# Performance work log

Hardware: AMD Instinct MI355X
Metric: run time of the kernel (lower is better)

The kernel has to match this reference:

```python
import jax, jax.numpy as jnp
import numpy as np

B, E, L, D = 64, 32, 512, 768
C1 = 1024
C2 = 1024
H = 8
EG = 32768
SPAN_H = 512
NLAB = 4


def setup_inputs() -> dict:
    key = jax.random.key(0)
    ks = jax.random.split(key, 48)
    def w(i, shape, s=0.02):
        return s * jax.random.normal(ks[i], shape, jnp.float32)
    N = B * E
    inp = {}
    inp['last_hidden'] = jax.random.normal(ks[0], (B, L, D), jnp.float32)
    mask = (jax.random.uniform(ks[1], (B, E, L)) < 0.25).astype(jnp.float32)
    inp['batch_edu_mask'] = mask.at[:, :, 0].set(1.0)  # every EDU has >=1 token
    inp['edu_lengths'] = jax.random.randint(ks[2], (B,), 1, E + 1)
    inp['batch_edge'] = jax.random.randint(ks[3], (2, EG), 0, N)
    inp['batch_edge_type'] = jax.random.randint(ks[4], (EG, 1), 0, 5).astype(jnp.float32)
    inp['batch_is_main'] = jax.random.randint(ks[5], (EG, 1), 0, 2).astype(jnp.float32)
    # span attention MLP
    inp['W1'] = w(6, (D, SPAN_H)); inp['b1'] = jnp.zeros((SPAN_H,), jnp.float32)
    inp['W2'] = w(7, (SPAN_H, 1)); inp['b2'] = jnp.zeros((1,), jnp.float32)
    # edge-attr embeddings (Linear(1, C))
    inp['Wr1'] = w(8, (1, C1)); inp['br1'] = jnp.zeros((C1,), jnp.float32)
    inp['Wm1'] = w(9, (1, C1)); inp['bm1'] = jnp.zeros((C1,), jnp.float32)
    inp['Wr2'] = w(10, (1, C2)); inp['br2'] = jnp.zeros((C2,), jnp.float32)
    inp['Wm2'] = w(11, (1, C2)); inp['bm2'] = jnp.zeros((C2,), jnp.float32)
    # TransformerConv 1: in=D, heads*out=C1, edge_dim=C1
    inp['q1W'] = w(12, (D, C1)); inp['q1b'] = jnp.zeros((C1,), jnp.float32)
    inp['k1W'] = w(13, (D, C1)); inp['k1b'] = jnp.zeros((C1,), jnp.float32)
    inp['v1W'] = w(14, (D, C1)); inp['v1b'] = jnp.zeros((C1,), jnp.float32)
    inp['e1W'] = w(15, (C1, C1))
    inp['s1W'] = w(16, (D, C1)); inp['s1b'] = jnp.zeros((C1,), jnp.float32)
    # TransformerConv 2: in=C1, heads*out=C2, edge_dim=C2
    inp['q2W'] = w(17, (C1, C2)); inp['q2b'] = jnp.zeros((C2,), jnp.float32)
    inp['k2W'] = w(18, (C1, C2)); inp['k2b'] = jnp.zeros((C2,), jnp.float32)
    inp['v2W'] = w(19, (C1, C2)); inp['v2b'] = jnp.zeros((C2,), jnp.float32)
    inp['e2W'] = w(20, (C2, C2))
    inp['s2W'] = w(21, (C1, C2)); inp['s2b'] = jnp.zeros((C2,), jnp.float32)
    inp['fcW'] = w(22, (C2, NLAB)); inp['fcb'] = jnp.zeros((NLAB,), jnp.float32)
    return inp


def _tconv(x, src, dst, edge_attr, Wq, bq, Wk, bk, Wv, bv, We, Ws, bs):
    # PyG TransformerConv (concat=True, beta=False, root_weight=True)
    N = x.shape[0]
    C = Wq.shape[1]
    d = C // H
    q = (x @ Wq + bq).reshape(N, H, d)              # [N,H,d]
    e = (edge_attr @ We).reshape(-1, H, d)          # [Eg,H,d] (lin_edge has no bias)
    k = (x @ Wk + bk)[src].reshape(-1, H, d) + e    # [Eg,H,d]
    v = (x @ Wv + bv)[src].reshape(-1, H, d) + e    # [Eg,H,d]
    logits = (q[dst] * k).sum(-1) / jnp.sqrt(jnp.float32(d))  # [Eg,H]
    m = jax.ops.segment_max(logits, dst, num_segments=N)
    ex = jnp.exp(logits - m[dst])
    den = jax.ops.segment_sum(ex, dst, num_segments=N)
    alpha = ex / den[dst]                            # scatter-softmax over dst
    agg = jax.ops.segment_sum(v * alpha[:, :, None], dst, num_segments=N).reshape(N, C)
    return agg + x @ Ws + bs                         # skip connection


def reference(last_hidden, batch_edu_mask, edu_lengths, batch_edge, batch_edge_type, batch_is_main,
              W1, b1, W2, b2,
              Wr1, br1, Wm1, bm1, Wr2, br2, Wm2, bm2,
              q1W, q1b, k1W, k1b, v1W, v1b, e1W, s1W, s1b,
              q2W, q2b, k2W, k2b, v2W, v2b, e2W, s2W, s2b,
              fcW, fcb):
    b = last_hidden.shape[0]
    # span extractor: masked softmax attention pooling per EDU
    att = jnp.maximum(last_hidden @ W1 + b1, 0.0) @ W2 + b2      # [B,L,1]
    logits = jnp.swapaxes(att, 1, 2) - 1e5 * (1.0 - batch_edu_mask)  # [B,E,L]
    probs = jax.nn.softmax(logits, axis=-1)
    edu = probs @ last_hidden                                     # [B,E,D]
    node = edu.reshape(-1, edu.shape[-1])                         # [B*E,D]
    src, dst = batch_edge[0], batch_edge[1]
    ea1 = batch_edge_type @ Wr1 + br1 + batch_is_main @ Wm1 + bm1
    node = _tconv(node, src, dst, ea1, q1W, q1b, k1W, k1b, v1W, v1b, e1W, s1W, s1b)
    ea2 = batch_edge_type @ Wr2 + br2 + batch_is_main @ Wm2 + bm2
    node = _tconv(node, src, dst, ea2, q2W, q2b, k2W, k2b, v2W, v2b, e2W, s2W, s2b)
    node = node.reshape(b, -1, node.shape[-1])                    # [B,E,C2]
    last_du = node[jnp.arange(b), edu_lengths - 1]                # [B,C2]
    return last_du @ fcW + fcb                                    # [B,NLAB]
```

## Files before the change

### kernel.cpp

```cpp
#include <hip/hip_runtime.h>
#include <math.h>
#include <stdint.h>

#define B_  64
#define E_  32
#define L_  512
#define D_  768
#define C_  1024
#define H_  8
#define EG_ 32768
#define SH_ 512
#define N_  2048
#define ND_ (N_ * D_)

typedef __bf16 bf16x8 __attribute__((ext_vector_type(8)));
typedef float f32x4 __attribute__((ext_vector_type(4)));
typedef unsigned short u16;
typedef u16 u16x4 __attribute__((ext_vector_type(4)));


__device__ __forceinline__ u16 bf16_rn(float x) {
  unsigned u = __builtin_bit_cast(unsigned, x);
  unsigned r = u + 0x7FFFu + ((u >> 16) & 1u);
  return (u16)(r >> 16);
}

__device__ __forceinline__ void gload16(const void* g, void* l) {
  __builtin_amdgcn_global_load_lds(
      (const __attribute__((address_space(1))) void*)(unsigned long long)(uintptr_t)g,
      (__attribute__((address_space(3))) void*)(unsigned int)(uintptr_t)l,
      16, 0, 0);
}

__global__ void k_wt9(const float* __restrict__ s0, const float* __restrict__ s1,
                      const float* __restrict__ s2, const float* __restrict__ s3,
                      const float* __restrict__ s4, const float* __restrict__ s5,
                      const float* __restrict__ s6, const float* __restrict__ s7,
                      const float* __restrict__ s8, u16* __restrict__ dstBase) {
  int x = blockIdx.x;
  const float* W; u16* TH; int K, Nc;
  if (x < 384) {
    W = s0; TH = dstBase; K = D_; Nc = SH_;
  } else if (x < 384 + 4 * 768) {
    int i = (x - 384) / 768; x = (x - 384) % 768;
    W = (i == 0) ? s1 : (i == 1) ? s2 : (i == 2) ? s3 : s4;
    TH = dstBase + SH_ * D_ + (size_t)i * C_ * D_; K = D_; Nc = C_;
  } else {
    int i = (x - 3456) / 1024; x = (x - 3456) % 1024;
    W = (i == 0) ? s5 : (i == 1) ? s6 : (i == 2) ? s7 : s8;
    TH = dstBase + SH_ * D_ + 4 * (size_t)C_ * D_ + (size_t)i * C_ * C_; K = C_; Nc = C_;
  }
  __shared__ float Ts[32][33];
  int nbk = K >> 5;
  int bk = x % nbk, bn = x / nbk;
  int tid = threadIdx.x;
  int tx = tid & 31, ty = tid >> 5;
  for (int r = ty; r < 32; r += 8)
    Ts[r][tx] = W[(size_t)(bk * 32 + r) * Nc + bn * 32 + tx];
  __syncthreads();
  for (int r = ty; r < 32; r += 8) {
    float v = Ts[tx][r];
    TH[(size_t)(bn * 32 + r) * K + bk * 32 + tx] = bf16_rn(v);
  }
}

__device__ __forceinline__ void gemm_core(
    const float* __restrict__ X, const u16* __restrict__ Bt,
    int K, int row0, int col0,
    u16* Ah, u16* Bh, f32x4 acc[4][4])
{
  int tid = threadIdx.x;
  int lane = tid & 63, w = tid >> 6;

  int aoff[4], boff[4];
#pragma unroll
  for (int i = 0; i < 4; i++) {
    int kc = lane >> 4;
    int rT = (w & 1) * 64 + i * 16 + (lane & 15);
    aoff[i] = rT * 128 + (((kc ^ (rT & 7)) & 7) << 4);
    int cT = (w >> 1) * 64 + i * 16 + (lane & 15);
    boff[i] = cT * 128 + (((kc ^ (cT & 7)) & 7) << 4);
  }

  int nkt = K >> 6;
  for (int kt = 0; kt < nkt; kt++) {
    int k0 = kt << 6;
    if (kt) __syncthreads();
#pragma unroll
    for (int p = 0; p < 8; p++) {
      int idx = tid + p * 256;
      int r = idx >> 4, c4 = idx & 15;
      float4 v = *(const float4*)&X[(size_t)(row0 + r) * K + k0 + c4 * 4];
      u16x4 hv = {bf16_rn(v.x), bf16_rn(v.y), bf16_rn(v.z), bf16_rn(v.w)};
      int off = r * 128 + ((((c4 >> 1) ^ (r & 7)) & 7) << 4) + (c4 & 1) * 8;
      *(u16x4*)((char*)Ah + off) = hv;
    }
#pragma unroll
    for (int q = 0; q < 4; q++) {
      int rT = w * 32 + q * 8 + (lane >> 3);
      int cs = (lane & 7) ^ (rT & 7);
      size_t gb = (size_t)(col0 + rT) * K + k0 + cs * 8;
      int lb = (w * 32 + q * 8) * 64;
      gload16(&Bt[gb], &Bh[lb]);
    }
    __syncthreads();
    bf16x8 ah0[4], ah1[4];
#pragma unroll
    for (int i = 0; i < 4; i++) {
      ah0[i] = *(const bf16x8*)((const char*)Ah + aoff[i]);
      ah1[i] = *(const bf16x8*)((const char*)Ah + (aoff[i] ^ 64));
    }
#pragma unroll
    for (int j = 0; j < 4; j++) {
      bf16x8 bh0 = *(const bf16x8*)((const char*)Bh + boff[j]);
#pragma unroll
      for (int i = 0; i < 4; i++)
        acc[i][j] = __builtin_amdgcn_mfma_f32_16x16x32_bf16(ah0[i], bh0, acc[i][j], 0, 0, 0);
      bf16x8 bh1 = *(const bf16x8*)((const char*)Bh + (boff[j] ^ 64));
#pragma unroll
      for (int i = 0; i < 4; i++)
        acc[i][j] = __builtin_amdgcn_mfma_f32_16x16x32_bf16(ah1[i], bh1, acc[i][j], 0, 0, 0);
    }
  }
}

__global__ __launch_bounds__(512, 2) void k_span_m(
    const float* __restrict__ lh, const u16* __restrict__ W1t,
    const float* __restrict__ b1, const float* __restrict__ W2,
    float* __restrict__ att) {
  __shared__ __align__(16) u16 Ah[64 * 64];
  __shared__ __align__(16) u16 Bh[512 * 64];
  int row0 = blockIdx.x * 64;
  int tid = threadIdx.x, lane = tid & 63, w = tid >> 6;

  f32x4 acc[4][4];
#pragma unroll
  for (int i = 0; i < 4; i++)
#pragma unroll
    for (int j = 0; j < 4; j++) acc[i][j] = (f32x4){0.f, 0.f, 0.f, 0.f};

  int kc = lane >> 4;
  int aoff[4], boff[4];
#pragma unroll
  for (int i = 0; i < 4; i++) {
    int rT = i * 16 + (lane & 15);
    aoff[i] = rT * 128 + (((kc ^ (rT & 7)) & 7) << 4);
  }
#pragma unroll
  for (int j = 0; j < 4; j++) {
    int cT = w * 64 + j * 16 + (lane & 15);
    boff[j] = cT * 128 + (((kc ^ (cT & 7)) & 7) << 4);
  }

  for (int kt = 0; kt < 12; kt++) {
    int k0 = kt << 6;
    if (kt) __syncthreads();
#pragma unroll
    for (int p = 0; p < 2; p++) {
      int idx = tid + p * 512;
      int r = idx >> 4, c4 = idx & 15;
      float4 v = *(const float4*)&lh[(size_t)(row0 + r) * D_ + k0 + c4 * 4];
      u16x4 hv = {bf16_rn(v.x), bf16_rn(v.y), bf16_rn(v.z), bf16_rn(v.w)};
      int off = r * 128 + ((((c4 >> 1) ^ (r & 7)) & 7) << 4) + (c4 & 1) * 8;
      *(u16x4*)((char*)Ah + off) = hv;
    }
#pragma unroll
    for (int q = 0; q < 8; q++) {
      int rT = w * 64 + q * 8 + (lane >> 3);
      int cs = (lane & 7) ^ (rT & 7);
      size_t gb = (size_t)rT * D_ + k0 + cs * 8;
      int lb = (w * 64 + q * 8) * 64;
      gload16(&W1t[gb], &Bh[lb]);
    }
    __syncthreads();
    bf16x8 ah0[4], ah1[4];
#pragma unroll
    for (int i = 0; i < 4; i++) {
      ah0[i] = *(const bf16x8*)((const char*)Ah + aoff[i]);
      ah1[i] = *(const bf16x8*)((const char*)Ah + (aoff[i] ^ 64));
    }
#pragma unroll
    for (int j = 0; j < 4; j++) {
      bf16x8 bh0 = *(const bf16x8*)((const char*)Bh + boff[j]);
#pragma unroll
      for (int i = 0; i < 4; i++)
        acc[i][j] = __builtin_amdgcn_mfma_f32_16x16x32_bf16(ah0[i], bh0, acc[i][j], 0, 0, 0);
      bf16x8 bh1 = *(const bf16x8*)((const char*)Bh + (boff[j] ^ 64));
#pragma unroll
      for (int i = 0; i < 4; i++)
        acc[i][j] = __builtin_amdgcn_mfma_f32_16x16x32_bf16(ah1[i], bh1, acc[i][j], 0, 0, 0);
    }
  }

  float b1v[4], w2v[4];
#pragma unroll
  for (int j = 0; j < 4; j++) {
    int col = w * 64 + j * 16 + (lane & 15);
    b1v[j] = b1[col]; w2v[j] = W2[col];
  }
  __syncthreads();
  float* sred = (float*)Ah;
#pragma unroll
  for (int i = 0; i < 4; i++) {
#pragma unroll
    for (int r = 0; r < 4; r++) {
      float s = 0.f;
#pragma unroll
      for (int j = 0; j < 4; j++) {
        float h = acc[i][j][r] + b1v[j];
        s += fmaxf(h, 0.f) * w2v[j];
      }
      s += __shfl_xor(s, 1); s += __shfl_xor(s, 2);
      s += __shfl_xor(s, 4); s += __shfl_xor(s, 8);
      if ((lane & 15) == 0)
        sred[w * 64 + i * 16 + (lane >> 4) * 4 + r] = s;
    }
  }
  __syncthreads();
  if (tid < 64) {
    float s = 0.f;
#pragma unroll
    for (int p = 0; p < 8; p++) s += sred[p * 64 + tid];
    att[row0 + tid] = s;
  }
}

__global__ void k_probs(const float* __restrict__ att, const float* __restrict__ b2,
                        const float* __restrict__ mask, float* __restrict__ pr) {
  int bi = blockIdx.x >> 2, eg = blockIdx.x & 3;
  int tid = threadIdx.x, lane = tid & 63, w = tid >> 6;
  __shared__ float att_s[512];
  float b2v = b2[0];
  int r0 = bi * 512 + tid;
  att_s[tid] = att[r0] + b2v;
  att_s[tid + 256] = att[r0 + 256] + b2v;
  __syncthreads();
#pragma unroll
  for (int it = 0; it < 2; it++) {
    int e = eg * 8 + it * 4 + w;
    const float* mrow = &mask[(size_t)(bi * E_ + e) * L_];
    float4 m0 = *(const float4*)&mrow[lane * 8];
    float4 m1 = *(const float4*)&mrow[lane * 8 + 4];
    float4 a0 = *(const float4*)&att_s[lane * 8];
    float4 a1 = *(const float4*)&att_s[lane * 8 + 4];
    float v[8];
    v[0] = a0.x - 1e5f * (1.f - m0.x); v[1] = a0.y - 1e5f * (1.f - m0.y);
    v[2] = a0.z - 1e5f * (1.f - m0.z); v[3] = a0.w - 1e5f * (1.f - m0.w);
    v[4] = a1.x - 1e5f * (1.f - m1.x); v[5] = a1.y - 1e5f * (1.f - m1.y);
    v[6] = a1.z - 1e5f * (1.f - m1.z); v[7] = a1.w - 1e5f * (1.f - m1.w);
    float mx = v[0];
#pragma unroll
    for (int i = 1; i < 8; i++) mx = fmaxf(mx, v[i]);
#pragma unroll
    for (int o = 32; o; o >>= 1) mx = fmaxf(mx, __shfl_xor(mx, o));
    float s = 0.f;
#pragma unroll
    for (int i = 0; i < 8; i++) { v[i] = expf(v[i] - mx); s += v[i]; }
#pragma unroll
    for (int o = 32; o; o >>= 1) s += __shfl_xor(s, o);
    float inv = 1.f / s;
    float4 o0 = {v[0] * inv, v[1] * inv, v[2] * inv, v[3] * inv};
    float4 o1 = {v[4] * inv, v[5] * inv, v[6] * inv, v[7] * inv};
    float* prow = &pr[(size_t)(bi * E_ + e) * L_];
    *(float4*)&prow[lane * 8] = o0;
    *(float4*)&prow[lane * 8 + 4] = o1;
  }
}

__global__ __launch_bounds__(256) void k_pool_m(const float* __restrict__ lh,
    const float* __restrict__ pr, float* __restrict__ node0) {
  __shared__ __align__(16) u16 As[32 * 32];
  __shared__ __align__(16) u16 Bs[32 * 128];
  int bi = blockIdx.x / 6, dc = blockIdx.x % 6;
  int col0 = dc * 128;
  int tid = threadIdx.x, lane = tid & 63, w = tid >> 6;
  const float* lhb = lh + (size_t)bi * L_ * D_;
  const float* prb = pr + (size_t)bi * E_ * L_;

  f32x4 acc[2][2];
#pragma unroll
  for (int m = 0; m < 2; m++)
#pragma unroll
    for (int c = 0; c < 2; c++) acc[m][c] = (f32x4){0.f, 0.f, 0.f, 0.f};

  int aoff[2];
#pragma unroll
  for (int m = 0; m < 2; m++) {
    int kc = lane >> 4;
    int e = m * 16 + (lane & 15);
    aoff[m] = e * 64 + (((kc ^ ((e >> 1) & 3)) & 3) << 4);
  }
  int se = tid >> 3, sk4 = tid & 7;
  int saoff = se * 64 + ((((sk4 >> 1) ^ ((se >> 1) & 3)) & 3) << 4) + (sk4 & 1) * 8;

  for (int kt = 0; kt < 16; kt++) {
    int l0 = kt << 5;
    if (kt) __syncthreads();
    {
      float4 v = *(const float4*)&prb[(size_t)se * L_ + l0 + sk4 * 4];
      u16x4 hv = {bf16_rn(v.x), bf16_rn(v.y), bf16_rn(v.z), bf16_rn(v.w)};
      *(u16x4*)((char*)As + saoff) = hv;
    }
#pragma unroll
    for (int p = 0; p < 4; p++) {
      int idx = tid + p * 256;
      int k = idx >> 5, c4 = idx & 31;
      float4 v = *(const float4*)&lhb[(size_t)(l0 + k) * D_ + col0 + c4 * 4];
      u16x4 hv = {bf16_rn(v.x), bf16_rn(v.y), bf16_rn(v.z), bf16_rn(v.w)};
      *(u16x4*)&Bs[k * 128 + c4 * 4] = hv;
    }
    __syncthreads();
    bf16x8 af[2];
#pragma unroll
    for (int m = 0; m < 2; m++)
      af[m] = *(const bf16x8*)((const char*)As + aoff[m]);
#pragma unroll
    for (int c = 0; c < 2; c++) {
      int colT = w * 32 + c * 16 + (lane & 15);
      int kg = (lane >> 4) * 8;
      union { bf16x8 v; u16 u[8]; } bb;
#pragma unroll
      for (int j = 0; j < 8; j++) bb.u[j] = Bs[(kg + j) * 128 + colT];
#pragma unroll
      for (int m = 0; m < 2; m++)
        acc[m][c] = __builtin_amdgcn_mfma_f32_16x16x32_bf16(af[m], bb.v, acc[m][c], 0, 0, 0);
    }
  }
#pragma unroll
  for (int m = 0; m < 2; m++)
#pragma unroll
    for (int c = 0; c < 2; c++) {
      int col = col0 + w * 32 + c * 16 + (lane & 15);
#pragma unroll
      for (int r = 0; r < 4; r++) {
        int e = m * 16 + (lane >> 4) * 4 + r;
        node0[(size_t)(bi * E_ + e) * D_ + col] = acc[m][c][r];
      }
    }
}

__global__ __launch_bounds__(256) void k_gemm4_m(
    const float* __restrict__ X, int K,
    const u16* __restrict__ Wt,
    const float* __restrict__ bb0, const float* __restrict__ bb1,
    const float* __restrict__ bb2, const float* __restrict__ bb3,
    float* __restrict__ O0, float* __restrict__ O1,
    float* __restrict__ O2, float* __restrict__ O3) {
  __shared__ __align__(16) u16 Ah[128 * 64], Bh[128 * 64];
  int rb = blockIdx.x & 15, cbm = blockIdx.x >> 4;
  int mat = cbm >> 3;
  int col0 = (cbm & 7) * 128, row0 = rb * 128;
  const u16* Bt = Wt + (size_t)mat * C_ * K;
  const float* bias; float* O;
  if (mat == 0)      { bias = bb0; O = O0; }
  else if (mat == 1) { bias = bb1; O = O1; }
  else if (mat == 2) { bias = bb2; O = O2; }
  else               { bias = bb3; O = O3; }

  f32x4 acc[4][4];
#pragma unroll
  for (int i = 0; i < 4; i++)
#pragma unroll
    for (int j = 0; j < 4; j++) acc[i][j] = (f32x4){0.f, 0.f, 0.f, 0.f};
  gemm_core(X, Bt, K, row0, col0, Ah, Bh, acc);

  int lane = threadIdx.x & 63, w = threadIdx.x >> 6;
  int wrow = (w & 1) * 64, wcol = (w >> 1) * 64;
#pragma unroll
  for (int j = 0; j < 4; j++) {
    int col = col0 + wcol + j * 16 + (lane & 15);
    float bv = bias[col];
#pragma unroll
    for (int i = 0; i < 4; i++) {
      int rowb = row0 + wrow + i * 16 + (lane >> 4) * 4;
#pragma unroll
      for (int r = 0; r < 4; r++)
        O[(size_t)(rowb + r) * C_ + col] = acc[i][j][r] + bv;
    }
  }
}

__global__ void k_combo2(const float* __restrict__ Wr1, const float* __restrict__ br1,
                         const float* __restrict__ Wm1, const float* __restrict__ bm1,
                         const float* __restrict__ e1W,
                         const float* __restrict__ Wr2, const float* __restrict__ br2,
                         const float* __restrict__ Wm2, const float* __restrict__ bm2,
                         const float* __restrict__ e2W,
                         float* __restrict__ e1c, float* __restrict__ e2c) {
  int x = blockIdx.x;
  int conv = x >> 6;
  int jb = x & 3, kb = (x >> 2) & 15;
  const float *Wr, *br, *Wm, *bm, *eW; float* out;
  if (conv == 0) { Wr = Wr1; br = br1; Wm = Wm1; bm = bm1; eW = e1W; out = e1c; }
  else           { Wr = Wr2; br = br2; Wm = Wm2; bm = bm2; eW = e2W; out = e2c; }
  int tid = threadIdx.x;
  __shared__ float sw[3][64];
  int k0 = kb * 64;
  if (tid < 64) {
    sw[0][tid] = Wr[k0 + tid];
    sw[1][tid] = Wm[k0 + tid];
    sw[2][tid] = br[k0 + tid] + bm[k0 + tid];
  }
  __syncthreads();
  int j = jb * 256 + tid;
  float a0 = 0.f, a1 = 0.f, a2 = 0.f;
#pragma unroll 8
  for (int kk = 0; kk < 64; kk++) {
    float w = eW[(size_t)(k0 + kk) * C_ + j];
    a0 += sw[0][kk] * w; a1 += sw[1][kk] * w; a2 += sw[2][kk] * w;
  }
#pragma unroll
  for (int c = 0; c < 10; c++)
    atomicAdd(&out[c * C_ + j], (float)(c >> 1) * a0 + (float)(c & 1) * a1 + a2);
}

__global__ void k_count(const int* __restrict__ dst, int* __restrict__ cnt) {
  int eg = blockIdx.x * 256 + threadIdx.x;
  atomicAdd(&cnt[dst[eg]], 1);
}

__global__ void k_scan(const int* __restrict__ cnt, int* __restrict__ off) {
  __shared__ int part[256];
  int t = threadIdx.x;
  int local[8]; int s = 0;
#pragma unroll
  for (int i = 0; i < 8; i++) { local[i] = cnt[t * 8 + i]; s += local[i]; }
  part[t] = s;
  __syncthreads();
  if (t == 0) {
    int r = 0;
    for (int i = 0; i < 256; i++) { int v = part[i]; part[i] = r; r += v; }
    off[N_] = r;
  }
  __syncthreads();
  int r = part[t];
#pragma unroll
  for (int i = 0; i < 8; i++) { off[t * 8 + i] = r; r += local[i]; }
}

__global__ void k_scatter(const int* __restrict__ dst, int* __restrict__ wcnt,
                          const int* __restrict__ off, int* __restrict__ perm) {
  int eg = blockIdx.x * 256 + threadIdx.x;
  int d = dst[eg];
  int p = atomicAdd(&wcnt[d], 1);
  perm[off[d] + p] = eg;
}

__global__ void k_agg(const float* __restrict__ q, const float* __restrict__ k,
                      const float* __restrict__ v, const float* __restrict__ ec,
                      const int* __restrict__ srcA, const float* __restrict__ etype,
                      const float* __restrict__ emain, const int* __restrict__ off,
                      const int* __restrict__ perm, float* __restrict__ O) {
  int dst = blockIdx.x;
  int beg = off[dst];
  int cntE = off[dst + 1] - beg;
  if (cntE == 0) return;
  if (cntE > 128) cntE = 128;
  int tid = threadIdx.x;
  __shared__ float lg[128][8];
  __shared__ int srcs[128];
  __shared__ int cids[128];
  for (int e = tid; e < cntE; e += 256) {
    int eg = perm[beg + e];
    srcs[e] = srcA[eg];
    cids[e] = ((int)(etype[eg] + 0.5f)) * 2 + (int)(emain[eg] + 0.5f);
  }
  __syncthreads();
  int c = tid * 4;
  int h = tid >> 5;
  float4 qv = *(const float4*)&q[dst * C_ + c];
  const float scale = 0.08838834764831845f;
  for (int e = 0; e < cntE; e++) {
    int s = srcs[e], ci = cids[e];
    float4 kv = *(const float4*)&k[s * C_ + c];
    float4 ev = *(const float4*)&ec[ci * C_ + c];
    float p = qv.x * (kv.x + ev.x) + qv.y * (kv.y + ev.y) +
              qv.z * (kv.z + ev.z) + qv.w * (kv.w + ev.w);
#pragma unroll
    for (int o = 16; o; o >>= 1) p += __shfl_xor(p, o);
    if ((tid & 31) == 0) lg[e][h] = p * scale;
  }
  __syncthreads();
  if (tid < 8) {
    float m = -1e30f;
    for (int e = 0; e < cntE; e++) m = fmaxf(m, lg[e][tid]);
    float ssum = 0.f;
    for (int e = 0; e < cntE; e++) { float x = expf(lg[e][tid] - m); lg[e][tid] = x; ssum += x; }
    float inv = 1.f / ssum;
    for (int e = 0; e < cntE; e++) lg[e][tid] *= inv;
  }
  __syncthreads();
  float4 acc = {0.f, 0.f, 0.f, 0.f};
  for (int e = 0; e < cntE; e++) {
    float a = lg[e][h];
    int s = srcs[e], ci = cids[e];
    float4 vv = *(const float4*)&v[s * C_ + c];
    float4 ev = *(const float4*)&ec[ci * C_ + c];
    acc.x += a * (vv.x + ev.x); acc.y += a * (vv.y + ev.y);
    acc.z += a * (vv.z + ev.z); acc.w += a * (vv.w + ev.w);
  }
  float4 o = *(const float4*)&O[dst * C_ + c];
  o.x += acc.x; o.y += acc.y; o.z += acc.z; o.w += acc.w;
  *(float4*)&O[dst * C_ + c] = o;
}

__global__ void k_final(const float* __restrict__ nB, const int* __restrict__ lens,
                        const float* __restrict__ fcW, const float* __restrict__ fcb,
                        float* __restrict__ out) {
  int b = blockIdx.x;
  int idx = lens[b] - 1;
  const float* row = &nB[(b * E_ + idx) * C_];
  int tid = threadIdx.x;
  int c = tid * 4;
  float4 r = *(const float4*)&row[c];
  float4 w0 = *(const float4*)&fcW[(c + 0) * 4];
  float4 w1 = *(const float4*)&fcW[(c + 1) * 4];
  float4 w2 = *(const float4*)&fcW[(c + 2) * 4];
  float4 w3 = *(const float4*)&fcW[(c + 3) * 4];
  float p0 = r.x * w0.x + r.y * w1.x + r.z * w2.x + r.w * w3.x;
  float p1 = r.x * w0.y + r.y * w1.y + r.z * w2.y + r.w * w3.y;
  float p2 = r.x * w0.z + r.y * w1.z + r.z * w2.z + r.w * w3.z;
  float p3 = r.x * w0.w + r.y * w1.w + r.z * w2.w + r.w * w3.w;
#pragma unroll
  for (int o = 32; o; o >>= 1) {
    p0 += __shfl_xor(p0, o); p1 += __shfl_xor(p1, o);
    p2 += __shfl_xor(p2, o); p3 += __shfl_xor(p3, o);
  }
  __shared__ float red[4][4];
  if ((tid & 63) == 0) {
    int w = tid >> 6;
    red[w][0] = p0; red[w][1] = p1; red[w][2] = p2; red[w][3] = p3;
  }
  __syncthreads();
  if (tid == 0) {
#pragma unroll
    for (int j = 0; j < 4; j++)
      out[b * 4 + j] = red[0][j] + red[1][j] + red[2][j] + red[3][j] + fcb[j];
  }
}

extern "C" void kernel_launch(void* const* d_in, const int* in_sizes, int n_in,
                              void* d_out, int out_size, void* d_ws, size_t ws_size,
                              hipStream_t stream) {
  (void)in_sizes; (void)n_in; (void)out_size; (void)ws_size;
  const float* lh    = (const float*)d_in[0];
  const float* mask  = (const float*)d_in[1];
  const int*   lens  = (const int*)d_in[2];
  const int*   edge  = (const int*)d_in[3];
  const float* etype = (const float*)d_in[4];
  const float* emain = (const float*)d_in[5];
  const float* W1   = (const float*)d_in[6];
  const float* b1   = (const float*)d_in[7];
  const float* W2   = (const float*)d_in[8];
  const float* b2   = (const float*)d_in[9];
  const float* Wr1  = (const float*)d_in[10];
  const float* br1  = (const float*)d_in[11];
  const float* Wm1  = (const float*)d_in[12];
  const float* bm1  = (const float*)d_in[13];
  const float* Wr2  = (const float*)d_in[14];
  const float* br2  = (const float*)d_in[15];
  const float* Wm2  = (const float*)d_in[16];
  const float* bm2  = (const float*)d_in[17];
  const float* q1W  = (const float*)d_in[18];
  const float* q1b  = (const float*)d_in[19];
  const float* k1W  = (const float*)d_in[20];
  const float* k1b  = (const float*)d_in[21];
  const float* v1W  = (const float*)d_in[22];
  const float* v1b  = (const float*)d_in[23];
  const float* e1W  = (const float*)d_in[24];
  const float* s1W  = (const float*)d_in[25];
  const float* s1b  = (const float*)d_in[26];
  const float* q2W  = (const float*)d_in[27];
  const float* q2b  = (const float*)d_in[28];
  const float* k2W  = (const float*)d_in[29];
  const float* k2b  = (const float*)d_in[30];
  const float* v2W  = (const float*)d_in[31];
  const float* v2b  = (const float*)d_in[32];
  const float* e2W  = (const float*)d_in[33];
  const float* s2W  = (const float*)d_in[34];
  const float* s2b  = (const float*)d_in[35];
  const float* fcW  = (const float*)d_in[36];
  const float* fcb  = (const float*)d_in[37];

  float* ws    = (float*)d_ws;
  float* att   = ws;
  float* node0 = att + 32768;
  float* e1c   = node0 + ND_;
  float* e2c   = e1c + 10 * 1024;
  float* qb    = e2c + 10 * 1024;
  float* kb    = qb + N_ * C_;
  float* vb    = kb + N_ * C_;
  float* nA    = vb + N_ * C_;
  float* nBuf  = nA + N_ * C_;
  int* cnt  = (int*)(nBuf + N_ * C_);
  int* wcnt = cnt + N_;
  int* off  = wcnt + N_;
  int* perm = off + (N_ + 8);
  u16* wtb  = (u16*)(perm + EG_);
  u16* w1t  = wtb;
  u16* wt1  = w1t + SH_ * D_;
  u16* wt2  = wt1 + 4 * C_ * D_;

  float* pr   = qb;

  const int* srcA = edge;
  const int* dstA = edge + EG_;

  (void)hipMemsetAsync(cnt, 0, 2 * N_ * sizeof(int), stream);
  k_count<<<EG_ / 256, 256, 0, stream>>>(dstA, cnt);
  k_scan<<<1, 256, 0, stream>>>(cnt, off);
  k_scatter<<<EG_ / 256, 256, 0, stream>>>(dstA, wcnt, off, perm);

  k_wt9<<<384 + 4 * 768 + 4 * 1024, 256, 0, stream>>>(
      W1, q1W, k1W, v1W, s1W, q2W, k2W, v2W, s2W, wtb);

  k_span_m<<<512, 512, 0, stream>>>(lh, w1t, b1, W2, att);

  (void)hipMemsetAsync(e1c, 0, 20 * C_ * sizeof(float), stream);
  k_combo2<<<128, 256, 0, stream>>>(Wr1, br1, Wm1, bm1, e1W,
                                    Wr2, br2, Wm2, bm2, e2W, e1c, e2c);

  k_probs<<<256, 256, 0, stream>>>(att, b2, mask, pr);
  k_pool_m<<<384, 256, 0, stream>>>(lh, pr, node0);

  k_gemm4_m<<<512, 256, 0, stream>>>(node0, D_, wt1,
                                     q1b, k1b, v1b, s1b, qb, kb, vb, nA);
  k_agg<<<N_, 256, 0, stream>>>(qb, kb, vb, e1c, srcA, etype, emain, off, perm, nA);

  k_gemm4_m<<<512, 256, 0, stream>>>(nA, C_, wt2,
                                     q2b, k2b, v2b, s2b, qb, kb, vb, nBuf);
  k_agg<<<N_, 256, 0, stream>>>(qb, kb, vb, e2c, srcA, etype, emain, off, perm, nBuf);

  k_final<<<B_, 256, 0, stream>>>(nBuf, lens, fcW, fcb, (float*)d_out);
}
```

Measured before the change: 244.5 us.

## Store Q/K/V in bf16 and retile span GEMM into row/column halves

The Q/K/V projections are now written as bf16, and the edge-aggregation kernel reads them as bf16 and widens to float. This halves the bytes of the irregular gathers over source nodes. The span-attention GEMM now gives each block 128 rows by 256 columns instead of 64 rows by all 512, with two partial score buffers summed in k_probs. That cuts shared memory per block and raises the occupancy target to 6. The trade-off is extra rounding error in the attention logits and values.

```diff
diff --git a/kernel.cpp b/kernel.cpp
--- a/kernel.cpp
+++ b/kernel.cpp
@@ -23,6 +23,10 @@
   unsigned u = __builtin_bit_cast(unsigned, x);
   unsigned r = u + 0x7FFFu + ((u >> 16) & 1u);
   return (u16)(r >> 16);
+}
+
+__device__ __forceinline__ float bf2f(u16 u) {
+  return __builtin_bit_cast(float, (unsigned)u << 16);
 }
 
 __device__ __forceinline__ void gload16(const void* g, void* l) {
@@ -124,14 +128,16 @@
   }
 }
 
-__global__ __launch_bounds__(512, 2) void k_span_m(
+__global__ __launch_bounds__(512, 6) void k_span_m(
     const float* __restrict__ lh, const u16* __restrict__ W1t,
     const float* __restrict__ b1, const float* __restrict__ W2,
-    float* __restrict__ att) {
-  __shared__ __align__(16) u16 Ah[64 * 64];
-  __shared__ __align__(16) u16 Bh[512 * 64];
-  int row0 = blockIdx.x * 64;
+    float* __restrict__ att2) {
+  __shared__ __align__(16) u16 Ah[128 * 64];
+  __shared__ __align__(16) u16 Bh[256 * 64];
+  int rb = blockIdx.x >> 1, cb = blockIdx.x & 1;
+  int row0 = rb * 128, col0 = cb * 256;
   int tid = threadIdx.x, lane = tid & 63, w = tid >> 6;
+  int rh = w & 1, cq = w >> 1;
 
   f32x4 acc[4][4];
 #pragma unroll
@@ -143,12 +149,12 @@
   int aoff[4], boff[4];
 #pragma unroll
   for (int i = 0; i < 4; i++) {
-    int rT = i * 16 + (lane & 15);
+    int rT = rh * 64 + i * 16 + (lane & 15);
     aoff[i] = rT * 128 + (((kc ^ (rT & 7)) & 7) << 4);
   }
 #pragma unroll
   for (int j = 0; j < 4; j++) {
-    int cT = w * 64 + j * 16 + (lane & 15);
+    int cT = cq * 64 + j * 16 + (lane & 15);
     boff[j] = cT * 128 + (((kc ^ (cT & 7)) & 7) << 4);
   }
 
@@ -156,7 +162,7 @@
     int k0 = kt << 6;
     if (kt) __syncthreads();
 #pragma unroll
-    for (int p = 0; p < 2; p++) {
+    for (int p = 0; p < 4; p++) {
       int idx = tid + p * 512;
       int r = idx >> 4, c4 = idx & 15;
       float4 v = *(const float4*)&lh[(size_t)(row0 + r) * D_ + k0 + c4 * 4];
@@ -165,11 +171,11 @@
       *(u16x4*)((char*)Ah + off) = hv;
     }
 #pragma unroll
-    for (int q = 0; q < 8; q++) {
-      int rT = w * 64 + q * 8 + (lane >> 3);
+    for (int q = 0; q < 4; q++) {
+      int rT = w * 32 + q * 8 + (lane >> 3);
       int cs = (lane & 7) ^ (rT & 7);
-      size_t gb = (size_t)rT * D_ + k0 + cs * 8;
-      int lb = (w * 64 + q * 8) * 64;
+      size_t gb = (size_t)(col0 + rT) * D_ + k0 + cs * 8;
+      int lb = (w * 32 + q * 8) * 64;
       gload16(&W1t[gb], &Bh[lb]);
     }
     __syncthreads();
@@ -195,7 +201,7 @@
   float b1v[4], w2v[4];
 #pragma unroll
   for (int j = 0; j < 4; j++) {
-    int col = w * 64 + j * 16 + (lane & 15);
+    int col = col0 + cq * 64 + j * 16 + (lane & 15);
     b1v[j] = b1[col]; w2v[j] = W2[col];
   }
   __syncthreads();
@@ -213,27 +219,24 @@
       s += __shfl_xor(s, 1); s += __shfl_xor(s, 2);
       s += __shfl_xor(s, 4); s += __shfl_xor(s, 8);
       if ((lane & 15) == 0)
-        sred[w * 64 + i * 16 + (lane >> 4) * 4 + r] = s;
-    }
-  }
-  __syncthreads();
-  if (tid < 64) {
-    float s = 0.f;
-#pragma unroll
-    for (int p = 0; p < 8; p++) s += sred[p * 64 + tid];
-    att[row0 + tid] = s;
-  }
-}
-
-__global__ void k_probs(const float* __restrict__ att, const float* __restrict__ b2,
+        sred[cq * 128 + rh * 64 + i * 16 + (lane >> 4) * 4 + r] = s;
+    }
+  }
+  __syncthreads();
+  if (tid < 128)
+    att2[(size_t)cb * 32768 + row0 + tid] =
+        sred[tid] + sred[128 + tid] + sred[256 + tid] + sred[384 + tid];
+}
+
+__global__ void k_probs(const float* __restrict__ att2, const float* __restrict__ b2,
                         const float* __restrict__ mask, float* __restrict__ pr) {
   int bi = blockIdx.x >> 2, eg = blockIdx.x & 3;
   int tid = threadIdx.x, lane = tid & 63, w = tid >> 6;
   __shared__ float att_s[512];
   float b2v = b2[0];
   int r0 = bi * 512 + tid;
-  att_s[tid] = att[r0] + b2v;
-  att_s[tid + 256] = att[r0 + 256] + b2v;
+  att_s[tid]       = att2[r0] + att2[32768 + r0] + b2v;
+  att_s[tid + 256] = att2[r0 + 256] + att2[32768 + r0 + 256] + b2v;
   __syncthreads();
 #pragma unroll
   for (int it = 0; it < 2; it++) {
@@ -344,18 +347,18 @@
     const u16* __restrict__ Wt,
     const float* __restrict__ bb0, const float* __restrict__ bb1,
     const float* __restrict__ bb2, const float* __restrict__ bb3,
-    float* __restrict__ O0, float* __restrict__ O1,
-    float* __restrict__ O2, float* __restrict__ O3) {
+    u16* __restrict__ O0, u16* __restrict__ O1,
+    u16* __restrict__ O2, float* __restrict__ O3) {
   __shared__ __align__(16) u16 Ah[128 * 64], Bh[128 * 64];
   int rb = blockIdx.x & 15, cbm = blockIdx.x >> 4;
   int mat = cbm >> 3;
   int col0 = (cbm & 7) * 128, row0 = rb * 128;
   const u16* Bt = Wt + (size_t)mat * C_ * K;
-  const float* bias; float* O;
-  if (mat == 0)      { bias = bb0; O = O0; }
-  else if (mat == 1) { bias = bb1; O = O1; }
-  else if (mat == 2) { bias = bb2; O = O2; }
-  else               { bias = bb3; O = O3; }
+  const float* bias;
+  if (mat == 0)      bias = bb0;
+  else if (mat == 1) bias = bb1;
+  else if (mat == 2) bias = bb2;
+  else               bias = bb3;
 
   f32x4 acc[4][4];
 #pragma unroll
@@ -366,16 +369,32 @@
 
   int lane = threadIdx.x & 63, w = threadIdx.x >> 6;
   int wrow = (w & 1) * 64, wcol = (w >> 1) * 64;
-#pragma unroll
-  for (int j = 0; j < 4; j++) {
-    int col = col0 + wcol + j * 16 + (lane & 15);
-    float bv = bias[col];
-#pragma unroll
-    for (int i = 0; i < 4; i++) {
-      int rowb = row0 + wrow + i * 16 + (lane >> 4) * 4;
-#pragma unroll
-      for (int r = 0; r < 4; r++)
-        O[(size_t)(rowb + r) * C_ + col] = acc[i][j][r] + bv;
+  if (mat < 3) {
+    u16* O = (mat == 0) ? O0 : (mat == 1) ? O1 : O2;
+#pragma unroll
+    for (int j = 0; j < 4; j++) {
+      int col = col0 + wcol + j * 16 + (lane & 15);
+      float bv = bias[col];
+#pragma unroll
+      for (int i = 0; i < 4; i++) {
+        int rowb = row0 + wrow + i * 16 + (lane >> 4) * 4;
+#pragma unroll
+        for (int r = 0; r < 4; r++)
+          O[(size_t)(rowb + r) * C_ + col] = bf16_rn(acc[i][j][r] + bv);
+      }
+    }
+  } else {
+#pragma unroll
+    for (int j = 0; j < 4; j++) {
+      int col = col0 + wcol + j * 16 + (lane & 15);
+      float bv = bias[col];
+#pragma unroll
+      for (int i = 0; i < 4; i++) {
+        int rowb = row0 + wrow + i * 16 + (lane >> 4) * 4;
+#pragma unroll
+        for (int r = 0; r < 4; r++)
+          O3[(size_t)(rowb + r) * C_ + col] = acc[i][j][r] + bv;
+      }
     }
   }
 }
@@ -446,8 +465,8 @@
   perm[off[d] + p] = eg;
 }
 
-__global__ void k_agg(const float* __restrict__ q, const float* __restrict__ k,
-                      const float* __restrict__ v, const float* __restrict__ ec,
+__global__ void k_agg(const u16* __restrict__ q, const u16* __restrict__ k,
+                      const u16* __restrict__ v, const float* __restrict__ ec,
                       const int* __restrict__ srcA, const float* __restrict__ etype,
                       const float* __restrict__ emain, const int* __restrict__ off,
                       const int* __restrict__ perm, float* __restrict__ O) {
@@ -468,14 +487,15 @@
   __syncthreads();
   int c = tid * 4;
   int h = tid >> 5;
-  float4 qv = *(const float4*)&q[dst * C_ + c];
+  ushort4 q4 = *(const ushort4*)&q[(size_t)dst * C_ + c];
+  float qx = bf2f(q4.x), qy = bf2f(q4.y), qz = bf2f(q4.z), qw = bf2f(q4.w);
   const float scale = 0.08838834764831845f;
   for (int e = 0; e < cntE; e++) {
     int s = srcs[e], ci = cids[e];
-    float4 kv = *(const float4*)&k[s * C_ + c];
+    ushort4 k4 = *(const ushort4*)&k[(size_t)s * C_ + c];
     float4 ev = *(const float4*)&ec[ci * C_ + c];
-    float p = qv.x * (kv.x + ev.x) + qv.y * (kv.y + ev.y) +
-              qv.z * (kv.z + ev.z) + qv.w * (kv.w + ev.w);
+    float p = qx * (bf2f(k4.x) + ev.x) + qy * (bf2f(k4.y) + ev.y) +
+              qz * (bf2f(k4.z) + ev.z) + qw * (bf2f(k4.w) + ev.w);
 #pragma unroll
     for (int o = 16; o; o >>= 1) p += __shfl_xor(p, o);
     if ((tid & 31) == 0) lg[e][h] = p * scale;
@@ -494,14 +514,14 @@
   for (int e = 0; e < cntE; e++) {
     float a = lg[e][h];
     int s = srcs[e], ci = cids[e];
-    float4 vv = *(const float4*)&v[s * C_ + c];
+    ushort4 v4 = *(const ushort4*)&v[(size_t)s * C_ + c];
     float4 ev = *(const float4*)&ec[ci * C_ + c];
-    acc.x += a * (vv.x + ev.x); acc.y += a * (vv.y + ev.y);
-    acc.z += a * (vv.z + ev.z); acc.w += a * (vv.w + ev.w);
-  }
-  float4 o = *(const float4*)&O[dst * C_ + c];
+    acc.x += a * (bf2f(v4.x) + ev.x); acc.y += a * (bf2f(v4.y) + ev.y);
+    acc.z += a * (bf2f(v4.z) + ev.z); acc.w += a * (bf2f(v4.w) + ev.w);
+  }
+  float4 o = *(const float4*)&O[(size_t)dst * C_ + c];
   o.x += acc.x; o.y += acc.y; o.z += acc.z; o.w += acc.w;
-  *(float4*)&O[dst * C_ + c] = o;
+  *(float4*)&O[(size_t)dst * C_ + c] = o;
 }
 
 __global__ void k_final(const float* __restrict__ nB, const int* __restrict__ lens,
@@ -583,25 +603,25 @@
   const float* fcb  = (const float*)d_in[37];
 
   float* ws    = (float*)d_ws;
-  float* att   = ws;
-  float* node0 = att + 32768;
+  float* node0 = ws + 32768;
   float* e1c   = node0 + ND_;
   float* e2c   = e1c + 10 * 1024;
-  float* qb    = e2c + 10 * 1024;
-  float* kb    = qb + N_ * C_;
-  float* vb    = kb + N_ * C_;
-  float* nA    = vb + N_ * C_;
-  float* nBuf  = nA + N_ * C_;
-  int* cnt  = (int*)(nBuf + N_ * C_);
+  u16* qb16 = (u16*)(e2c + 10 * 1024);
+  u16* kb16 = qb16 + (size_t)N_ * C_;
+  u16* vb16 = kb16 + (size_t)N_ * C_;
+  float* nA   = (float*)(vb16 + (size_t)N_ * C_);
+  float* nBuf = nA + (size_t)N_ * C_;
+  int* cnt  = (int*)(nBuf + (size_t)N_ * C_);
   int* wcnt = cnt + N_;
   int* off  = wcnt + N_;
   int* perm = off + (N_ + 8);
   u16* wtb  = (u16*)(perm + EG_);
   u16* w1t  = wtb;
   u16* wt1  = w1t + SH_ * D_;
-  u16* wt2  = wt1 + 4 * C_ * D_;
-
-  float* pr   = qb;
+  u16* wt2  = wt1 + 4 * (size_t)C_ * D_;
+
+  float* pr   = (float*)qb16;
+  float* att2 = (float*)kb16;
 
   const int* srcA = edge;
   const int* dstA = edge + EG_;
@@ -614,22 +634,22 @@
   k_wt9<<<384 + 4 * 768 + 4 * 1024, 256, 0, stream>>>(
       W1, q1W, k1W, v1W, s1W, q2W, k2W, v2W, s2W, wtb);
 
-  k_span_m<<<512, 512, 0, stream>>>(lh, w1t, b1, W2, att);
+  k_span_m<<<512, 512, 0, stream>>>(lh, w1t, b1, W2, att2);
 
   (void)hipMemsetAsync(e1c, 0, 20 * C_ * sizeof(float), stream);
   k_combo2<<<128, 256, 0, stream>>>(Wr1, br1, Wm1, bm1, e1W,
                                     Wr2, br2, Wm2, bm2, e2W, e1c, e2c);
 
-  k_probs<<<256, 256, 0, stream>>>(att, b2, mask, pr);
+  k_probs<<<256, 256, 0, stream>>>(att2, b2, mask, pr);
   k_pool_m<<<384, 256, 0, stream>>>(lh, pr, node0);
 
   k_gemm4_m<<<512, 256, 0, stream>>>(node0, D_, wt1,
-                                     q1b, k1b, v1b, s1b, qb, kb, vb, nA);
-  k_agg<<<N_, 256, 0, stream>>>(qb, kb, vb, e1c, srcA, etype, emain, off, perm, nA);
+                                     q1b, k1b, v1b, s1b, qb16, kb16, vb16, nA);
+  k_agg<<<N_, 256, 0, stream>>>(qb16, kb16, vb16, e1c, srcA, etype, emain, off, perm, nA);
 
   k_gemm4_m<<<512, 256, 0, stream>>>(nA, C_, wt2,
-                                     q2b, k2b, v2b, s2b, qb, kb, vb, nBuf);
-  k_agg<<<N_, 256, 0, stream>>>(qb, kb, vb, e2c, srcA, etype, emain, off, perm, nBuf);
+                                     q2b, k2b, v2b, s2b, qb16, kb16, vb16, nBuf);
+  k_agg<<<N_, 256, 0, stream>>>(qb16, kb16, vb16, e2c, srcA, etype, emain, off, perm, nBuf);
 
   k_final<<<B_, 256, 0, stream>>>(nBuf, lens, fcW, fcb, (float*)d_out);
 }
```

New measurement: 393.0 us. 1.61x slower.
